# Kernel optimization log

Hardware: AMD Instinct MI355X
Metric: run time of the kernel (lower is better)

The kernel has to match this reference:

```python
import math
import jax, jax.numpy as jnp
import numpy as np

B, S, HID, NH = 8, 512, 1024, 16
D = HID // NH          # head dim = 64
SPAN = 512             # att_span = max_relative_positions = max_position_embeddings


def _linear(x, W, b):
    # torch nn.Linear: y = x @ W.T + b, W is [out, in]
    return jnp.einsum('...i,oi->...o', x, W) + b


def _heads(x):
    # [B, S, HID] -> [B, NH, S, D]
    b, s, _ = x.shape
    return x.reshape(b, s, NH, D).transpose(0, 2, 1, 3)


def setup_inputs() -> dict:
    key = jax.random.key(0)
    ks = jax.random.split(key, 16)
    f = lambda i, shape, sc=1.0: jax.random.normal(ks[i], shape, dtype=jnp.float32) * sc
    return {
        'q': f(0, (B, S, HID)),
        'k': f(1, (B, S, HID)),
        'v': f(2, (B, S, HID)),
        'attention_mask': jnp.tril(jnp.ones((S, S), dtype=bool))[None, None],  # causal [1,1,S,S]
        'Wq': f(3, (HID, HID), 0.02), 'bq': jnp.zeros((HID,), jnp.float32),
        'Wk': f(4, (HID, HID), 0.02), 'bk': jnp.zeros((HID,), jnp.float32),
        'Wv': f(5, (HID, HID), 0.02), 'bv': jnp.zeros((HID,), jnp.float32),
        'Wpk': f(6, (HID, HID), 0.02), 'bpk': jnp.zeros((HID,), jnp.float32),
        'Wpq': f(7, (HID, HID), 0.02), 'bpq': jnp.zeros((HID,), jnp.float32),
        'rel_emb': f(8, (2 * SPAN, HID), 0.02),
    }


def reference(q, k, v, attention_mask, Wq, bq, Wk, bk, Wv, bv, Wpk, bpk, Wpq, bpq, rel_emb):
    scale_factor = 3  # 1 (content) + c2p + p2c
    scale = 1.0 / math.sqrt(D * scale_factor)

    ql = _heads(_linear(q, Wq, bq))   # [B,NH,S,D]
    kl = _heads(_linear(k, Wk, bk))
    vl = _heads(_linear(v, Wv, bv))

    # content-to-content scores
    scores = jnp.einsum('bhqd,bhkd->bhqk', ql, kl) * scale

    # relative positions (no bucketing since position_buckets = -1)
    rel = jnp.arange(S)[:, None] - jnp.arange(S)[None, :]          # [S,S]
    c2p_pos = jnp.clip(rel + SPAN, 0, 2 * SPAN - 1)
    p2c_pos = jnp.clip(-rel + SPAN, 0, 2 * SPAN - 1)

    # projected relative-position embeddings -> [NH, 2*SPAN, D]
    pk = _linear(rel_emb, Wpk, bpk).reshape(2 * SPAN, NH, D).transpose(1, 0, 2)
    pq = _linear(rel_emb, Wpq, bpq).reshape(2 * SPAN, NH, D).transpose(1, 0, 2)

    # content-to-position: out[b,h,q,k] = (q . pos_key)[b,h,q, c2p_pos[q,k]]
    c2p = jnp.einsum('bhqd,hjd->bhqj', ql, pk) * scale             # [B,NH,S,2*SPAN]
    c2p = jnp.take_along_axis(c2p, jnp.broadcast_to(c2p_pos[None, None], (B, NH, S, S)), axis=-1)

    # position-to-content: gathered[b,h,k,q] = (k . pos_query)[b,h,k, p2c_pos[k,q]], then transpose
    p2c = jnp.einsum('bhkd,hjd->bhkj', kl, pq) * scale             # [B,NH,S,2*SPAN]
    p2c = jnp.take_along_axis(p2c, jnp.broadcast_to(p2c_pos[None, None], (B, NH, S, S)), axis=-1)

    scores = scores + c2p + jnp.swapaxes(p2c, -1, -2)
    # subtract detached row max (as in torch: .max(...).values.detach())
    scores = scores - jax.lax.stop_gradient(scores.max(axis=-1, keepdims=True))

    # XSoftmax: masked softmax, then zero masked positions
    neg = jnp.float32(-1e30)
    probs = jax.nn.softmax(jnp.where(attention_mask, scores, neg), axis=-1)
    probs = jnp.where(attention_mask, probs, 0.0)

    ctx = jnp.einsum('bhqk,bhkd->bhqd', probs, vl)                 # [B,NH,S,D]
    return ctx.transpose(0, 2, 1, 3).reshape(B, S, HID)
```

## Files before the change

### kernel.cpp

```cpp
#include <hip/hip_runtime.h>
#include <hip/hip_bf16.h>
#include <math.h>

#define SCALE 0.07216878364870323f
#define NEG_BIG -1e30f

typedef __attribute__((ext_vector_type(8))) short bf16x8;
typedef __attribute__((ext_vector_type(4))) short bf16x4;
typedef __attribute__((ext_vector_type(4))) float f32x4;
#define MFMA_BF16 __builtin_amdgcn_mfma_f32_16x16x32_bf16

#define BARX()   asm volatile("s_barrier" ::: "memory")
#define VMCNT2() asm volatile("s_waitcnt vmcnt(2)" ::: "memory")
#define VMCNT0() asm volatile("s_waitcnt vmcnt(0)" ::: "memory")

static __device__ __forceinline__ float bf2f(__hip_bfloat16 x) { return __bfloat162float(x); }
static __device__ __forceinline__ __hip_bfloat16 f2bf(float x) { return __float2bfloat16(x); }
static __device__ __forceinline__ short f2bs(float x) {
  union { __hip_bfloat16 b; short s; } u; u.b = __float2bfloat16(x); return u.s;
}
static __device__ __forceinline__ float s2f(short v) {
  union { float f; unsigned u; } x; x.u = ((unsigned)(unsigned short)v) << 16; return x.f;
}
static __device__ __forceinline__ bf16x4 cvt4(float4 f) {
  bf16x4 r; r[0] = f2bs(f.x); r[1] = f2bs(f.y); r[2] = f2bs(f.z); r[3] = f2bs(f.w);
  return r;
}
static __device__ __forceinline__ bf16x8 ldg8(const __hip_bfloat16* p) {
  return *(const bf16x8*)p;
}
static __device__ __forceinline__ void gl_lds16(const __hip_bfloat16* g, __hip_bfloat16* l) {
  __builtin_amdgcn_global_load_lds(
      (const __attribute__((address_space(1))) void*)g,
      (__attribute__((address_space(3))) void*)l, 16, 0, 0);
}

struct CvtJob { const float* src; __hip_bfloat16* dst; int n4; };
struct CvtArgs { CvtJob j[9]; };

__global__ __launch_bounds__(256) void cvt_kernel(CvtArgs a) {
  const CvtJob jb = a.j[blockIdx.y];
  const float4* s = (const float4*)jb.src;
  bf16x4* d = (bf16x4*)jb.dst;
  const int stride = gridDim.x * 256;
  for (int i = blockIdx.x * 256 + threadIdx.x; i < jb.n4; i += stride)
    d[i] = cvt4(s[i]);
}

struct Gemm { const __hip_bfloat16* A; const __hip_bfloat16* W;
              const float* bias; __hip_bfloat16* out; int mode; int mBits; int nBlk; };
struct ProjArgs { Gemm g[5]; };

static __device__ __forceinline__ void stage_half(const __hip_bfloat16* gtile,
                                                  __hip_bfloat16* ltile,
                                                  int half, int wave, int lane) {
  const int r = lane >> 3;
  const int chunk = (lane & 7) ^ r;
#pragma unroll
  for (int c = 0; c < 2; c++) {
    const int rowbase = half * 128 + c * 64 + wave * 8;
    gl_lds16(gtile + (size_t)(rowbase + r) * 1024 + chunk * 8,
             ltile + (size_t)rowbase * 64);
  }
}

__global__ __launch_bounds__(512, 2) void proj_kernel(ProjArgs pa) {
  const Gemm g = pa.g[blockIdx.y];
  if ((int)blockIdx.x >= g.nBlk) return;
  __shared__ __hip_bfloat16 As[2][256][64];
  __shared__ __hip_bfloat16 Ws[2][256][64];

  const int bid = blockIdx.x;
  const int m0 = (bid & ((1 << g.mBits) - 1)) * 256;
  const int n0 = (bid >> g.mBits) * 256;
  const int tid = threadIdx.x;
  const int wave = tid >> 6, lane = tid & 63;
  const int q16 = lane >> 4, l16 = lane & 15;
  const int wr = wave >> 2, wc = wave & 3;
  const int l7 = l16 & 7;

  const __hip_bfloat16* Ag = g.A + (size_t)m0 * 1024;
  const __hip_bfloat16* Wg = g.W + (size_t)n0 * 1024;

  f32x4 acc[8][4] = {};

  stage_half(Ag, &As[0][0][0], 0, wave, lane);
  stage_half(Ag, &As[0][0][0], 1, wave, lane);
  stage_half(Wg, &Ws[0][0][0], 0, wave, lane);
  stage_half(Wg, &Ws[0][0][0], 1, wave, lane);
  stage_half(Ag + 64, &As[1][0][0], 0, wave, lane);
  VMCNT2();
  BARX();

  for (int t = 0; t < 16; ++t) {
    const int cur = t & 1;
    const __hip_bfloat16* Ac = &As[cur][0][0];
    const __hip_bfloat16* Wc = &Ws[cur][0][0];
    __hip_bfloat16* An = &As[cur ^ 1][0][0];
    __hip_bfloat16* Wn = &Ws[cur ^ 1][0][0];
    const __hip_bfloat16* gAn = Ag + (size_t)(t + 1) * 64;
    const __hip_bfloat16* gWn = Wg + (size_t)(t + 1) * 64;
    const bool pf = (t + 1 < 16);

#pragma unroll
    for (int kh = 0; kh < 2; kh++) {
      const int csw = ((kh * 4 + q16) ^ l7) * 8;
      bf16x8 bw[4];
#pragma unroll
      for (int ni = 0; ni < 4; ni++)
        bw[ni] = *(const bf16x8*)(Wc + (size_t)(wc * 64 + ni * 16 + l16) * 64 + csw);
#pragma unroll
      for (int mh = 0; mh < 2; mh++) {
        bf16x8 af[4];
#pragma unroll
        for (int mi = 0; mi < 4; mi++)
          af[mi] = *(const bf16x8*)(Ac + (size_t)(wr * 128 + mh * 64 + mi * 16 + l16) * 64 + csw);
        const int ph = kh * 2 + mh;
        if (pf) {
          if (ph == 0)      stage_half(gAn, An, 1, wave, lane);
          else if (ph == 1) stage_half(gWn, Wn, 0, wave, lane);
          else if (ph == 2) stage_half(gWn, Wn, 1, wave, lane);
        }
        __builtin_amdgcn_s_setprio(1);
#pragma unroll
        for (int ni = 0; ni < 4; ni++)
#pragma unroll
          for (int mi = 0; mi < 4; mi++)
            acc[mh * 4 + mi][ni] =
                MFMA_BF16(af[mi], bw[ni], acc[mh * 4 + mi][ni], 0, 0, 0);
        __builtin_amdgcn_s_setprio(0);
      }
    }
    BARX();
    if (t + 2 < 16) {
      stage_half(Ag + (size_t)(t + 2) * 64, &As[cur][0][0], 0, wave, lane);
      VMCNT2();
    } else {
      VMCNT0();
    }
    BARX();
  }

#pragma unroll
  for (int ni = 0; ni < 4; ni++) {
    const int n = n0 + wc * 64 + ni * 16 + l16;
#pragma unroll
    for (int mi = 0; mi < 8; mi++) {
#pragma unroll
      for (int rr = 0; rr < 4; rr++) {
        const int m = m0 + wr * 128 + mi * 16 + q16 * 4 + rr;
        float val = acc[mi][ni][rr];
        size_t oidx;
        if (g.mode == 0) {
          val += g.bias[n];
          const int b = m >> 9, s = m & 511;
          const int h = n >> 6, d = n & 63;
          oidx = ((size_t)((b * 16 + h) * 512 + s)) * 64 + d;
        } else if (g.mode == 1) {
          val += g.bias[m];
          const int b = n >> 9, s = n & 511;
          const int h = m >> 6, d = m & 63;
          oidx = ((size_t)((b * 16 + h) * 64 + d)) * 512 + s;
        } else {
          val += g.bias[n];
          const int h = n >> 6, d = n & 63;
          oidx = ((size_t)(h * 512 + m)) * 64 + d;
        }
        g.out[oidx] = f2bf(val);
      }
    }
  }
}

__global__ __launch_bounds__(256) void attn_kernel(
    const __hip_bfloat16* __restrict__ ql,
    const __hip_bfloat16* __restrict__ kl,
    const __hip_bfloat16* __restrict__ vlT,
    const __hip_bfloat16* __restrict__ pk,
    const __hip_bfloat16* __restrict__ pq,
    float* __restrict__ out)
{
  __shared__ float rowsum[32];
  __shared__ __align__(16) __hip_bfloat16 sc[32][520];
  __shared__ __align__(16) __hip_bfloat16 ks_[32][72];
  __shared__ __align__(16) __hip_bfloat16 pks[32][72];
  __shared__ __align__(16) __hip_bfloat16 pqs[2][32][72];
  __shared__ __hip_bfloat16 cpb[2][32][34];
  __shared__ __align__(16) __hip_bfloat16 pqbT[2][2][32][36];

  const int bid = blockIdx.x;
  const int qt = 15 - (bid >> 7);
  const int bh = bid & 127;
  const int h = bh & 15, b = bh >> 4;
  const int q0 = qt * 32;

  const __hip_bfloat16* qlp = ql + (size_t)bh * 512 * 64;
  const __hip_bfloat16* klp = kl + (size_t)bh * 512 * 64;
  const __hip_bfloat16* vtp = vlT + (size_t)bh * 64 * 512;
  const __hip_bfloat16* pkp = pk + (size_t)h * 512 * 64;
  const __hip_bfloat16* pqp = pq + (size_t)h * 512 * 64;

  const int tid = threadIdx.x, wave = tid >> 6, lane = tid & 63;
  const int q16 = lane >> 4, l16 = lane & 15;
  const int wr = wave & 1, wc = wave >> 1;

  const int rowQ = q0 + wr * 16 + l16;
  bf16x8 aq0 = ldg8(qlp + (size_t)rowQ * 64 + q16 * 8);
  bf16x8 aq1 = ldg8(qlp + (size_t)rowQ * 64 + 32 + q16 * 8);

  {
    int4 z = {0, 0, 0, 0};
    *(int4*)(&pqs[1][tid >> 3][(tid & 7) * 8]) = z;
  }

  const int kEnd = q0 + 32;
  const int nIter = kEnd >> 5;

  const int sr = tid >> 3, sseg = tid & 7;
  int4 rKv, rPKv, rPQv;
  {
    rKv  = ((const int4*)(klp + (size_t)(q0 + sr) * 64))[sseg];
    rPKv = ((const int4*)(pkp + (size_t)(0 + sr) * 64))[sseg];
    rPQv = ((const int4*)(pqp + (size_t)(0 + sr) * 64))[sseg];
  }

  f32x4 qkPrev = {};
  int k0Prev = 0, parPrev = 0;

  for (int it = 0; it < nIter; ++it) {
    const int k0 = q0 - it * 32;
    const int par = it & 1;
    __syncthreads();
    *(int4*)(&ks_[sr][sseg * 8]) = rKv;
    *(int4*)(&pks[sr][sseg * 8]) = rPKv;
    *(int4*)(&pqs[par][sr][sseg * 8]) = rPQv;
    if (it > 0) {
#pragma unroll
      for (int rr = 0; rr < 4; rr++) {
        const int qh = wr * 16 + q16 * 4 + rr;
        const int kh = wc * 16 + l16;
        if (k0Prev + kh > q0 + qh) {
          sc[qh][k0Prev + kh] = f2bf(NEG_BIG);
        } else {
          const int dlt = qh - kh;
          const float c2pv = (dlt >= 0) ? bf2f(cpb[parPrev][qh][dlt])
                                        : bf2f(cpb[parPrev ^ 1][qh][dlt + 32]);
          const float p2cv = (dlt >= 0) ? bf2f(pqbT[parPrev][1][dlt][kh])
                                        : bf2f(pqbT[parPrev][0][dlt + 32][kh]);
          float v = (qkPrev[rr] + c2pv + p2cv) * SCALE;
          v = fminf(v, 60.f); v = fmaxf(v, -60.f);
          sc[qh][k0Prev + kh] = f2bf(v);
        }
      }
    }
    __syncthreads();
    if (it + 1 < nIter) {
      const int k0n = k0 - 32, jbn = q0 - k0n;
      rKv  = ((const int4*)(klp + (size_t)(k0n + sr) * 64))[sseg];
      rPKv = ((const int4*)(pkp + (size_t)(jbn + sr) * 64))[sseg];
      rPQv = ((const int4*)(pqp + (size_t)(jbn + sr) * 64))[sseg];
    }

    const int rA = wr * 16 + l16;
    const int rB = wc * 16 + l16;
    f32x4 qk = {}, cp = {}, p0 = {}, p1 = {};
#pragma unroll
    for (int ksi = 0; ksi < 2; ksi++) {
      const int ko = ksi * 32 + q16 * 8;
      bf16x8 aq = ksi ? aq1 : aq0;
      bf16x8 ak = *(const bf16x8*)(&ks_[rA][ko]);
      bf16x8 bk = *(const bf16x8*)(&ks_[rB][ko]);
      bf16x8 bp = *(const bf16x8*)(&pks[rB][ko]);
      bf16x8 b1 = *(const bf16x8*)(&pqs[par][rB][ko]);
      bf16x8 b0 = *(const bf16x8*)(&pqs[par ^ 1][rB][ko]);
      qk = MFMA_BF16(aq, bk, qk, 0, 0, 0);
      cp = MFMA_BF16(aq, bp, cp, 0, 0, 0);
      p0 = MFMA_BF16(ak, b0, p0, 0, 0, 0);
      p1 = MFMA_BF16(ak, b1, p1, 0, 0, 0);
    }
    {
      const int cw = wc * 16 + l16;
      const int rwb = wr * 16 + q16 * 4;
      bf16x4 v0, v1;
#pragma unroll
      for (int rr = 0; rr < 4; rr++) {
        cpb[par][rwb + rr][cw] = f2bf(cp[rr]);
        v0[rr] = f2bs(p0[rr]);
        v1[rr] = f2bs(p1[rr]);
      }
      *(bf16x4*)(&pqbT[par][0][cw][rwb]) = v0;
      *(bf16x4*)(&pqbT[par][1][cw][rwb]) = v1;
    }
    qkPrev = qk; k0Prev = k0; parPrev = par;
  }
  __syncthreads();
  {
#pragma unroll
    for (int rr = 0; rr < 4; rr++) {
      const int qh = wr * 16 + q16 * 4 + rr;
      const int kh = wc * 16 + l16;
      if (k0Prev + kh > q0 + qh) {
        sc[qh][k0Prev + kh] = f2bf(NEG_BIG);
      } else {
        const int dlt = qh - kh;
        const float c2pv = (dlt >= 0) ? bf2f(cpb[parPrev][qh][dlt])
                                      : bf2f(cpb[parPrev ^ 1][qh][dlt + 32]);
        const float p2cv = (dlt >= 0) ? bf2f(pqbT[parPrev][1][dlt][kh])
                                      : bf2f(pqbT[parPrev][0][dlt + 32][kh]);
        float v = (qkPrev[rr] + c2pv + p2cv) * SCALE;
        v = fminf(v, 60.f); v = fmaxf(v, -60.f);
        sc[qh][k0Prev + kh] = f2bf(v);
      }
    }
  }
  __syncthreads();

  {
    const int row = tid >> 3, sub = tid & 7;
    float m = NEG_BIG;
    for (int c = sub * 8; c < kEnd; c += 64) {
      bf16x8 x8 = *(const bf16x8*)(&sc[row][c]);
#pragma unroll
      for (int e = 0; e < 8; e++) m = fmaxf(m, s2f(x8[e]));
    }
    for (int off = 1; off < 8; off <<= 1) m = fmaxf(m, __shfl_xor(m, off));
    float s = 0.f;
    for (int c = sub * 8; c < kEnd; c += 64) {
      bf16x8 x8 = *(const bf16x8*)(&sc[row][c]);
      bf16x8 p8;
#pragma unroll
      for (int e = 0; e < 8; e++) {
        const float p = __expf(s2f(x8[e]) - m);
        p8[e] = f2bs(p);
        s += p;
      }
      *(bf16x8*)(&sc[row][c]) = p8;
    }
    for (int off = 1; off < 8; off <<= 1) s += __shfl_xor(s, off);
    if (sub == 0) rowsum[row] = s;
  }

  f32x4 octx[2] = {};
  __hip_bfloat16 (*vt)[72] = (__hip_bfloat16 (*)[72])(&pqs[0][0][0]);
  for (int k0 = 0; k0 < kEnd; k0 += 64) {
    __syncthreads();
    {
      const int r = tid >> 2, seg = tid & 3;
      const int4* src = (const int4*)(vtp + (size_t)r * 512 + k0);
      *(int4*)(&vt[r][seg * 8])       = src[seg];
      *(int4*)(&vt[r][(seg + 4) * 8]) = src[seg + 4];
    }
    __syncthreads();
#pragma unroll
    for (int sub = 0; sub < 2; sub++) {
      const int kk = k0 + sub * 32;
      if (kk < kEnd) {
        bf16x8 af = *(const bf16x8*)(&sc[wr * 16 + l16][kk + q16 * 8]);
#pragma unroll
        for (int cs = 0; cs < 2; cs++) {
          bf16x8 bv = *(const bf16x8*)(&vt[wc * 32 + cs * 16 + l16][sub * 32 + q16 * 8]);
          octx[cs] = MFMA_BF16(af, bv, octx[cs], 0, 0, 0);
        }
      }
    }
  }

  for (int cs = 0; cs < 2; cs++) {
    const int d = wc * 32 + cs * 16 + l16;
    for (int rr = 0; rr < 4; rr++) {
      const int qh = wr * 16 + q16 * 4 + rr;
      const float val = octx[cs][rr] / rowsum[qh];
      out[((size_t)(b * 512 + q0 + qh)) * 1024 + h * 64 + d] = val;
    }
  }
}

extern "C" void kernel_launch(void* const* d_in, const int* in_sizes, int n_in,
                              void* d_out, int out_size, void* d_ws, size_t ws_size,
                              hipStream_t stream) {
  const float* q   = (const float*)d_in[0];
  const float* k   = (const float*)d_in[1];
  const float* v   = (const float*)d_in[2];
  const float* Wq  = (const float*)d_in[4];
  const float* bq  = (const float*)d_in[5];
  const float* Wk  = (const float*)d_in[6];
  const float* bk  = (const float*)d_in[7];
  const float* Wv  = (const float*)d_in[8];
  const float* bv  = (const float*)d_in[9];
  const float* Wpk = (const float*)d_in[10];
  const float* bpk = (const float*)d_in[11];
  const float* Wpq = (const float*)d_in[12];
  const float* bpq = (const float*)d_in[13];
  const float* rel = (const float*)d_in[14];
  float* out = (float*)d_out;

  char* ws = (char*)d_ws;
  const size_t MB = 1u << 20;
  __hip_bfloat16* bqi  = (__hip_bfloat16*)(ws);
  __hip_bfloat16* bki  = (__hip_bfloat16*)(ws + 8 * MB);
  __hip_bfloat16* bvi  = (__hip_bfloat16*)(ws + 16 * MB);
  __hip_bfloat16* bWq  = (__hip_bfloat16*)(ws + 24 * MB);
  __hip_bfloat16* bWk  = (__hip_bfloat16*)(ws + 26 * MB);
  __hip_bfloat16* bWv  = (__hip_bfloat16*)(ws + 28 * MB);
  __hip_bfloat16* bWpk = (__hip_bfloat16*)(ws + 30 * MB);
  __hip_bfloat16* bWpq = (__hip_bfloat16*)(ws + 32 * MB);
  __hip_bfloat16* brel = (__hip_bfloat16*)(ws + 34 * MB);
  __hip_bfloat16* wql  = (__hip_bfloat16*)(ws + 35 * MB);
  __hip_bfloat16* wkl  = (__hip_bfloat16*)(ws + 43 * MB);
  __hip_bfloat16* wvlT = (__hip_bfloat16*)(ws + 51 * MB);
  __hip_bfloat16* wpk  = (__hip_bfloat16*)(ws + 59 * MB);
  __hip_bfloat16* wpq  = (__hip_bfloat16*)(ws + 60 * MB);

  CvtArgs ca;
  ca.j[0] = { q,   bqi,  4194304 / 4 };
  ca.j[1] = { k,   bki,  4194304 / 4 };
  ca.j[2] = { v,   bvi,  4194304 / 4 };
  ca.j[3] = { Wq,  bWq,  1048576 / 4 };
  ca.j[4] = { Wk,  bWk,  1048576 / 4 };
  ca.j[5] = { Wv,  bWv,  1048576 / 4 };
  ca.j[6] = { Wpk, bWpk, 1048576 / 4 };
  ca.j[7] = { Wpq, bWpq, 1048576 / 4 };
  ca.j[8] = { rel + (size_t)512 * 1024, brel, 524288 / 4 };
  cvt_kernel<<<dim3(1024, 9), 256, 0, stream>>>(ca);

  ProjArgs pj;
  pj.g[0] = { bqi,  bWq,  bq,  wql,  0, 4, 64 };
  pj.g[1] = { bki,  bWk,  bk,  wkl,  0, 4, 64 };
  pj.g[2] = { bWv,  bvi,  bv,  wvlT, 1, 2, 64 };
  pj.g[3] = { brel, bWpk, bpk, wpk,  2, 1, 8 };
  pj.g[4] = { brel, bWpq, bpq, wpq,  2, 1, 8 };
  proj_kernel<<<dim3(64, 5), 512, 0, stream>>>(pj);

  attn_kernel<<<2048, 256, 0, stream>>>(wql, wkl, wvlT, wpk, wpq, out);
}
```

Baseline: 242.0 us.

## Fold softmax scale into projections, triple-buffer attention tiles, fuse row max

The softmax scale is folded into the Q and pos-query projection epilogues, which removes the per-score multiply in attention. The K/PK/PQ tiles and c2p buffers are double- or triple-buffered, so one barrier per iteration can be removed and the next global loads are issued earlier. The row max is tracked in registers during score assembly and reduced via shuffles plus LDS, replacing a full rescan of the score row. MFMA sections are wrapped in s_setprio, and the V staging loop is double-buffered to drop a barrier; the extra LDS footprint may reduce occupancy.

```diff
diff --git a/kernel.cpp b/kernel.cpp
--- a/kernel.cpp
+++ b/kernel.cpp
@@ -48,7 +48,8 @@
 }
 
 struct Gemm { const __hip_bfloat16* A; const __hip_bfloat16* W;
-              const float* bias; __hip_bfloat16* out; int mode; int mBits; int nBlk; };
+              const float* bias; __hip_bfloat16* out; int mode; int mBits; int nBlk;
+              float oscale; };
 struct ProjArgs { Gemm g[5]; };
 
 static __device__ __forceinline__ void stage_half(const __hip_bfloat16* gtile,
@@ -152,17 +153,17 @@
         float val = acc[mi][ni][rr];
         size_t oidx;
         if (g.mode == 0) {
-          val += g.bias[n];
+          val = (val + g.bias[n]) * g.oscale;
           const int b = m >> 9, s = m & 511;
           const int h = n >> 6, d = n & 63;
           oidx = ((size_t)((b * 16 + h) * 512 + s)) * 64 + d;
         } else if (g.mode == 1) {
-          val += g.bias[m];
+          val = (val + g.bias[m]) * g.oscale;
           const int b = n >> 9, s = n & 511;
           const int h = m >> 6, d = m & 63;
           oidx = ((size_t)((b * 16 + h) * 64 + d)) * 512 + s;
         } else {
-          val += g.bias[n];
+          val = (val + g.bias[n]) * g.oscale;
           const int h = n >> 6, d = n & 63;
           oidx = ((size_t)(h * 512 + m)) * 64 + d;
         }
@@ -180,13 +181,13 @@
     const __hip_bfloat16* __restrict__ pq,
     float* __restrict__ out)
 {
+  __shared__ __align__(16) __hip_bfloat16 pool[2][64][72];
+  __shared__ __align__(16) __hip_bfloat16 sc[32][520];
+  __shared__ __align__(16) __hip_bfloat16 pqs3[3][32][72];
+  __shared__ __align__(16) __hip_bfloat16 cpb3[3][32][34];
+  __shared__ __align__(16) __hip_bfloat16 pqbT2[2][2][32][36];
+  __shared__ float mred[2][32];
   __shared__ float rowsum[32];
-  __shared__ __align__(16) __hip_bfloat16 sc[32][520];
-  __shared__ __align__(16) __hip_bfloat16 ks_[32][72];
-  __shared__ __align__(16) __hip_bfloat16 pks[32][72];
-  __shared__ __align__(16) __hip_bfloat16 pqs[2][32][72];
-  __shared__ __hip_bfloat16 cpb[2][32][34];
-  __shared__ __align__(16) __hip_bfloat16 pqbT[2][2][32][36];
 
   const int bid = blockIdx.x;
   const int qt = 15 - (bid >> 7);
@@ -210,7 +211,7 @@
 
   {
     int4 z = {0, 0, 0, 0};
-    *(int4*)(&pqs[1][tid >> 3][(tid & 7) * 8]) = z;
+    *(int4*)(&pqs3[2][tid >> 3][(tid & 7) * 8]) = z;
   }
 
   const int kEnd = q0 + 32;
@@ -226,14 +227,22 @@
 
   f32x4 qkPrev = {};
   int k0Prev = 0, parPrev = 0;
+  int s3c = 0, s3p = 2, s3pp = 1;
+  float mloc[4] = {NEG_BIG, NEG_BIG, NEG_BIG, NEG_BIG};
 
   for (int it = 0; it < nIter; ++it) {
     const int k0 = q0 - it * 32;
     const int par = it & 1;
+    *(int4*)(&pool[par][sr][sseg * 8])      = rKv;
+    *(int4*)(&pool[par][32 + sr][sseg * 8]) = rPKv;
+    *(int4*)(&pqs3[s3c][sr][sseg * 8])      = rPQv;
     __syncthreads();
-    *(int4*)(&ks_[sr][sseg * 8]) = rKv;
-    *(int4*)(&pks[sr][sseg * 8]) = rPKv;
-    *(int4*)(&pqs[par][sr][sseg * 8]) = rPQv;
+    if (it + 1 < nIter) {
+      const int k0n = k0 - 32, jbn = q0 - k0n;
+      rKv  = ((const int4*)(klp + (size_t)(k0n + sr) * 64))[sseg];
+      rPKv = ((const int4*)(pkp + (size_t)(jbn + sr) * 64))[sseg];
+      rPQv = ((const int4*)(pqp + (size_t)(jbn + sr) * 64))[sseg];
+    }
     if (it > 0) {
 #pragma unroll
       for (int rr = 0; rr < 4; rr++) {
@@ -243,55 +252,52 @@
           sc[qh][k0Prev + kh] = f2bf(NEG_BIG);
         } else {
           const int dlt = qh - kh;
-          const float c2pv = (dlt >= 0) ? bf2f(cpb[parPrev][qh][dlt])
-                                        : bf2f(cpb[parPrev ^ 1][qh][dlt + 32]);
-          const float p2cv = (dlt >= 0) ? bf2f(pqbT[parPrev][1][dlt][kh])
-                                        : bf2f(pqbT[parPrev][0][dlt + 32][kh]);
-          float v = (qkPrev[rr] + c2pv + p2cv) * SCALE;
+          const float c2pv = (dlt >= 0) ? bf2f(cpb3[s3p][qh][dlt])
+                                        : bf2f(cpb3[s3pp][qh][dlt + 32]);
+          const float p2cv = (dlt >= 0) ? bf2f(pqbT2[parPrev][1][dlt][kh])
+                                        : bf2f(pqbT2[parPrev][0][dlt + 32][kh]);
+          float v = qkPrev[rr] + c2pv + p2cv;
           v = fminf(v, 60.f); v = fmaxf(v, -60.f);
+          mloc[rr] = fmaxf(mloc[rr], v);
           sc[qh][k0Prev + kh] = f2bf(v);
         }
       }
-    }
-    __syncthreads();
-    if (it + 1 < nIter) {
-      const int k0n = k0 - 32, jbn = q0 - k0n;
-      rKv  = ((const int4*)(klp + (size_t)(k0n + sr) * 64))[sseg];
-      rPKv = ((const int4*)(pkp + (size_t)(jbn + sr) * 64))[sseg];
-      rPQv = ((const int4*)(pqp + (size_t)(jbn + sr) * 64))[sseg];
     }
 
     const int rA = wr * 16 + l16;
     const int rB = wc * 16 + l16;
     f32x4 qk = {}, cp = {}, p0 = {}, p1 = {};
+    __builtin_amdgcn_s_setprio(1);
 #pragma unroll
     for (int ksi = 0; ksi < 2; ksi++) {
       const int ko = ksi * 32 + q16 * 8;
       bf16x8 aq = ksi ? aq1 : aq0;
-      bf16x8 ak = *(const bf16x8*)(&ks_[rA][ko]);
-      bf16x8 bk = *(const bf16x8*)(&ks_[rB][ko]);
-      bf16x8 bp = *(const bf16x8*)(&pks[rB][ko]);
-      bf16x8 b1 = *(const bf16x8*)(&pqs[par][rB][ko]);
-      bf16x8 b0 = *(const bf16x8*)(&pqs[par ^ 1][rB][ko]);
+      bf16x8 ak = *(const bf16x8*)(&pool[par][rA][ko]);
+      bf16x8 bk = *(const bf16x8*)(&pool[par][rB][ko]);
+      bf16x8 bp = *(const bf16x8*)(&pool[par][32 + rB][ko]);
+      bf16x8 b1 = *(const bf16x8*)(&pqs3[s3c][rB][ko]);
+      bf16x8 b0 = *(const bf16x8*)(&pqs3[s3p][rB][ko]);
       qk = MFMA_BF16(aq, bk, qk, 0, 0, 0);
       cp = MFMA_BF16(aq, bp, cp, 0, 0, 0);
       p0 = MFMA_BF16(ak, b0, p0, 0, 0, 0);
       p1 = MFMA_BF16(ak, b1, p1, 0, 0, 0);
     }
+    __builtin_amdgcn_s_setprio(0);
     {
       const int cw = wc * 16 + l16;
       const int rwb = wr * 16 + q16 * 4;
       bf16x4 v0, v1;
 #pragma unroll
       for (int rr = 0; rr < 4; rr++) {
-        cpb[par][rwb + rr][cw] = f2bf(cp[rr]);
+        cpb3[s3c][rwb + rr][cw] = f2bf(cp[rr]);
         v0[rr] = f2bs(p0[rr]);
         v1[rr] = f2bs(p1[rr]);
       }
-      *(bf16x4*)(&pqbT[par][0][cw][rwb]) = v0;
-      *(bf16x4*)(&pqbT[par][1][cw][rwb]) = v1;
+      *(bf16x4*)(&pqbT2[par][0][cw][rwb]) = v0;
+      *(bf16x4*)(&pqbT2[par][1][cw][rwb]) = v1;
     }
     qkPrev = qk; k0Prev = k0; parPrev = par;
+    const int t3 = s3pp; s3pp = s3p; s3p = s3c; s3c = t3;
   }
   __syncthreads();
   {
@@ -303,27 +309,31 @@
         sc[qh][k0Prev + kh] = f2bf(NEG_BIG);
       } else {
         const int dlt = qh - kh;
-        const float c2pv = (dlt >= 0) ? bf2f(cpb[parPrev][qh][dlt])
-                                      : bf2f(cpb[parPrev ^ 1][qh][dlt + 32]);
-        const float p2cv = (dlt >= 0) ? bf2f(pqbT[parPrev][1][dlt][kh])
-                                      : bf2f(pqbT[parPrev][0][dlt + 32][kh]);
-        float v = (qkPrev[rr] + c2pv + p2cv) * SCALE;
+        const float c2pv = (dlt >= 0) ? bf2f(cpb3[s3p][qh][dlt])
+                                      : bf2f(cpb3[s3pp][qh][dlt + 32]);
+        const float p2cv = (dlt >= 0) ? bf2f(pqbT2[parPrev][1][dlt][kh])
+                                      : bf2f(pqbT2[parPrev][0][dlt + 32][kh]);
+        float v = qkPrev[rr] + c2pv + p2cv;
         v = fminf(v, 60.f); v = fmaxf(v, -60.f);
+        mloc[rr] = fmaxf(mloc[rr], v);
         sc[qh][k0Prev + kh] = f2bf(v);
       }
     }
+  }
+#pragma unroll
+  for (int rr = 0; rr < 4; rr++) {
+    float m = mloc[rr];
+    m = fmaxf(m, __shfl_xor(m, 1));
+    m = fmaxf(m, __shfl_xor(m, 2));
+    m = fmaxf(m, __shfl_xor(m, 4));
+    m = fmaxf(m, __shfl_xor(m, 8));
+    if (l16 == 0) mred[wc][wr * 16 + q16 * 4 + rr] = m;
   }
   __syncthreads();
 
   {
     const int row = tid >> 3, sub = tid & 7;
-    float m = NEG_BIG;
-    for (int c = sub * 8; c < kEnd; c += 64) {
-      bf16x8 x8 = *(const bf16x8*)(&sc[row][c]);
-#pragma unroll
-      for (int e = 0; e < 8; e++) m = fmaxf(m, s2f(x8[e]));
-    }
-    for (int off = 1; off < 8; off <<= 1) m = fmaxf(m, __shfl_xor(m, off));
+    const float m = fmaxf(mred[0][row], mred[1][row]);
     float s = 0.f;
     for (int c = sub * 8; c < kEnd; c += 64) {
       bf16x8 x8 = *(const bf16x8*)(&sc[row][c]);
@@ -341,27 +351,30 @@
   }
 
   f32x4 octx[2] = {};
-  __hip_bfloat16 (*vt)[72] = (__hip_bfloat16 (*)[72])(&pqs[0][0][0]);
-  for (int k0 = 0; k0 < kEnd; k0 += 64) {
-    __syncthreads();
-    {
-      const int r = tid >> 2, seg = tid & 3;
-      const int4* src = (const int4*)(vtp + (size_t)r * 512 + k0);
-      *(int4*)(&vt[r][seg * 8])       = src[seg];
-      *(int4*)(&vt[r][(seg + 4) * 8]) = src[seg + 4];
-    }
-    __syncthreads();
-#pragma unroll
-    for (int sub = 0; sub < 2; sub++) {
-      const int kk = k0 + sub * 32;
-      if (kk < kEnd) {
-        bf16x8 af = *(const bf16x8*)(&sc[wr * 16 + l16][kk + q16 * 8]);
-#pragma unroll
-        for (int cs = 0; cs < 2; cs++) {
-          bf16x8 bv = *(const bf16x8*)(&vt[wc * 32 + cs * 16 + l16][sub * 32 + q16 * 8]);
-          octx[cs] = MFMA_BF16(af, bv, octx[cs], 0, 0, 0);
+  {
+    int p = 0;
+    for (int k0 = 0; k0 < kEnd; k0 += 64, p ^= 1) {
+      {
+        const int r = tid >> 2, seg = tid & 3;
+        const int4* src = (const int4*)(vtp + (size_t)r * 512 + k0);
+        *(int4*)(&pool[p][r][seg * 8])       = src[seg];
+        *(int4*)(&pool[p][r][(seg + 4) * 8]) = src[seg + 4];
+      }
+      __syncthreads();
+      __builtin_amdgcn_s_setprio(1);
+#pragma unroll
+      for (int sub = 0; sub < 2; sub++) {
+        const int kk = k0 + sub * 32;
+        if (kk < kEnd) {
+          bf16x8 af = *(const bf16x8*)(&sc[wr * 16 + l16][kk + q16 * 8]);
+#pragma unroll
+          for (int cs = 0; cs < 2; cs++) {
+            bf16x8 bv = *(const bf16x8*)(&pool[p][wc * 32 + cs * 16 + l16][sub * 32 + q16 * 8]);
+            octx[cs] = MFMA_BF16(af, bv, octx[cs], 0, 0, 0);
+          }
         }
       }
+      __builtin_amdgcn_s_setprio(0);
     }
   }
 
@@ -424,11 +437,11 @@
   cvt_kernel<<<dim3(1024, 9), 256, 0, stream>>>(ca);
 
   ProjArgs pj;
-  pj.g[0] = { bqi,  bWq,  bq,  wql,  0, 4, 64 };
-  pj.g[1] = { bki,  bWk,  bk,  wkl,  0, 4, 64 };
-  pj.g[2] = { bWv,  bvi,  bv,  wvlT, 1, 2, 64 };
-  pj.g[3] = { brel, bWpk, bpk, wpk,  2, 1, 8 };
-  pj.g[4] = { brel, bWpq, bpq, wpq,  2, 1, 8 };
+  pj.g[0] = { bqi,  bWq,  bq,  wql,  0, 4, 64, SCALE };
+  pj.g[1] = { bki,  bWk,  bk,  wkl,  0, 4, 64, 1.0f };
+  pj.g[2] = { bWv,  bvi,  bv,  wvlT, 1, 2, 64, 1.0f };
+  pj.g[3] = { brel, bWpk, bpk, wpk,  2, 1, 8,  1.0f };
+  pj.g[4] = { brel, bWpq, bpq, wpq,  2, 1, 8,  SCALE };
   proj_kernel<<<dim3(64, 5), 512, 0, stream>>>(pj);
 
   attn_kernel<<<2048, 256, 0, stream>>>(wql, wkl, wvlT, wpk, wpq, out);
```

Result: no change. 241.2 us (-0.3%).
